# Performance work log

Measured on AMD Instinct MI355X. Metric: run time of the kernel, lower is better.

## Reference

```python
import jax, jax.numpy as jnp
import numpy as np

N_NODES = 100000
N_EDGES = 800000
VOCAB = 256      # node_dict_size
NODE_DIM = 256
HIDDEN = 256
N_MASK = 10000


def setup_inputs() -> dict:
    key = jax.random.key(0)
    ks = jax.random.split(key, 8)
    return {
        "x": jax.random.randint(ks[0], (N_NODES, 1), 0, VOCAB, dtype=jnp.int64 if jax.config.jax_enable_x64 else jnp.int32),
        "edge_index": jax.random.randint(ks[1], (2, N_EDGES), 0, N_NODES, dtype=jnp.int32),
        "mask_x_position": jax.random.randint(ks[2], (N_MASK,), 0, N_NODES, dtype=jnp.int32),
        "emb": jax.random.normal(ks[3], (VOCAB, NODE_DIM), dtype=jnp.float32) * (NODE_DIM ** -0.5),
        "W1": jax.random.normal(ks[4], (NODE_DIM, HIDDEN), dtype=jnp.float32) * (NODE_DIM ** -0.5),
        "b1": jnp.zeros((HIDDEN,), dtype=jnp.float32),
        "W2": jax.random.normal(ks[5], (HIDDEN, VOCAB), dtype=jnp.float32) * (HIDDEN ** -0.5),
        "b2": jnp.zeros((VOCAB,), dtype=jnp.float32),
    }


def _gcn_conv(h, W, b, src, dst, norm, n_nodes):
    # PyG GCNConv: out = scatter_add(norm * (h @ W)[src], dst) + b
    hw = h @ W                                      # [N, out]
    msgs = hw[src] * norm[:, None]                  # [E+N, out]
    out = jax.ops.segment_sum(msgs, dst, num_segments=n_nodes)
    return out + b


def _gcn_norm(edge_index, n_nodes):
    # add self-loops, compute sym-normalized edge weights (PyG gcn_norm)
    loops = jnp.arange(n_nodes, dtype=edge_index.dtype)
    src = jnp.concatenate([edge_index[0], loops])
    dst = jnp.concatenate([edge_index[1], loops])
    deg = jax.ops.segment_sum(jnp.ones_like(dst, dtype=jnp.float32), dst,
                              num_segments=n_nodes)  # in-degree incl. self-loop
    dinv = jnp.where(deg > 0, jax.lax.rsqrt(deg), 0.0)
    norm = dinv[src] * dinv[dst]                    # [E+N]
    return src, dst, norm


def reference(x, edge_index, mask_x_position, emb, W1, b1, W2, b2):
    n_nodes = x.shape[0]
    src, dst, norm = _gcn_norm(edge_index, n_nodes)
    h = emb[x[:, 0]]                                # Embedding + squeeze(1) -> [N, node_dim]
    # dropout p=0 / eval mode -> identity
    h = _gcn_conv(h, W1, b1, src, dst, norm, n_nodes)
    h = jax.nn.relu(h)
    h = _gcn_conv(h, W2, b2, src, dst, norm, n_nodes)  # [N, vocab]
    return jax.nn.log_softmax(h[mask_x_position], axis=1)
```

## Files before the change

### kernel.cpp

```cpp
#include <hip/hip_runtime.h>
#include <stdint.h>

#define NN 100000
#define NE 800000
#define ND 256
#define NM 10000
#define NMP 10048
#define NTOT (NN + NM)
#define NTB ((NTOT + 1023) / 1024)
#define NPB 128
#define NBK 782
#define BCAP 1280
#define TILE 1024
#define EBK ((NE + TILE - 1) / TILE)

typedef __attribute__((ext_vector_type(8))) short bf16x8;
typedef __attribute__((ext_vector_type(4))) float f32x4;

__device__ __forceinline__ float bf2f(unsigned short u) {
    return __uint_as_float(((unsigned)u) << 16);
}
__device__ __forceinline__ unsigned short f2bf(float f) {
    unsigned u = __float_as_uint(f);
    u += 0x7fffu + ((u >> 16) & 1u);
    return (unsigned short)(u >> 16);
}


__global__ void k_maskmap(const int* __restrict__ mpos, int* __restrict__ minfo,
                          int* __restrict__ flag, int* __restrict__ gcur,
                          int* __restrict__ nctr) {
    int j = blockIdx.x * 256 + threadIdx.x;
    if (j < NM) {
        int p = mpos[j];
        minfo[p] = (j + 1) << 1;
        flag[p] = 1;
    }
    if (j < NBK) gcur[j] = j * BCAP;
    if (j == 0) *nctr = 0;
}

__global__ __launch_bounds__(256) void k_bin(
    const int* __restrict__ src, const int* __restrict__ dst,
    const int* __restrict__ minfo, int* __restrict__ flag,
    int* __restrict__ gcur, int* __restrict__ ebuf,
    const float* __restrict__ emb, const float* __restrict__ W1,
    const float* __restrict__ W2,
    unsigned short* __restrict__ M1, unsigned short* __restrict__ W2t) {
    __shared__ int lcnt[NBK];
    __shared__ int sd[TILE], ss[TILE];
    __shared__ float er[ND];
    int b = blockIdx.x, t = threadIdx.x;
    if (b >= EBK) {
        int bb = b - EBK;
        if (bb < ND) {
            er[t] = emb[bb * ND + t];
            __syncthreads();
            float acc = 0.f;
            for (int k = 0; k < ND; k++) acc += er[k] * W1[k * ND + t];
            M1[bb * ND + t] = f2bf(acc);
        } else {
            int n = bb - ND;
            W2t[n * ND + t] = f2bf(W2[t * ND + n]);
        }
        return;
    }
    for (int i = t; i < NBK; i += 256) lcnt[i] = 0;
    __syncthreads();
    int e0 = b * TILE;
#pragma unroll
    for (int k = 0; k < TILE / 256; k++) {
        int idx = t + k * 256;
        int e = e0 + idx;
        if (e < NE) {
            int d = dst[e], s = src[e];
            sd[idx] = d; ss[idx] = s;
            atomicAdd(&lcnt[d >> 7], 1);
            if (minfo[d] > 0) atomicExch(&flag[s], 1);
        }
    }
    __syncthreads();
    for (int i = t; i < NBK; i += 256) {
        int c = lcnt[i];
        lcnt[i] = c ? atomicAdd(&gcur[i], c) : 0;
    }
    __syncthreads();
    int nv = min(NE - e0, TILE);
#pragma unroll
    for (int k = 0; k < TILE / 256; k++) {
        int idx = t + k * 256;
        if (idx < nv) {
            int d = sd[idx], s = ss[idx];
            int bk = d >> 7, j = d & 127;
            int pos = atomicAdd(&lcnt[bk], 1);
            if (pos < (bk + 1) * BCAP) ebuf[pos] = s | (j << 17);
        }
    }
}

__global__ void k_bhist(const int* __restrict__ gcur, const int* __restrict__ ebuf,
                        int* __restrict__ carr) {
    __shared__ int bins[NPB];
    int b = blockIdx.x, t = threadIdx.x;
    if (t < NPB) bins[t] = 0;
    __syncthreads();
    int n = min(gcur[b] - b * BCAP, BCAP);
    int base = b * BCAP;
    for (int i = t; i < n; i += 256)
        atomicAdd(&bins[ebuf[base + i] >> 17], 1);
    __syncthreads();
    int node = b * NPB + t;
    if (t < NPB && node < NN) carr[node] = bins[t];
}

__global__ void k_scanA(int* __restrict__ carr, int* __restrict__ part,
                        const int* __restrict__ x, const int* __restrict__ flag,
                        const int* __restrict__ mpos,
                        int4* __restrict__ xd4,
                        int* __restrict__ nctr, int* __restrict__ nlist) {
    int b = blockIdx.x, t = threadIdx.x;
    int base = b * 1024 + t * 4;
    int s = 0;
#pragma unroll
    for (int k = 0; k < 4; k++) {
        int i = base + k;
        if (i < NTOT) {
            int c;
            if (i < NN) {
                c = carr[i];
                float dv = rsqrtf((float)c + 1.0f);
                int cc = 0;
                if (flag[i] == 1) {
                    cc = atomicAdd(nctr, 1);
                    nlist[cc] = i;
                }
                xd4[i] = make_int4(x[i], __float_as_int(dv), cc, 0);
            } else {
                c = carr[mpos[i - NN]];
                carr[i] = c;
            }
            s += c;
        }
    }
    int lane = t & 63, wv = t >> 6;
    int xx = s;
    for (int o = 1; o < 64; o <<= 1) { int y = __shfl_up(xx, o, 64); if (lane >= o) xx += y; }
    __shared__ int ws[4];
    if (lane == 63) ws[wv] = xx;
    __syncthreads();
    if (t == 0) part[b] = ws[0] + ws[1] + ws[2] + ws[3];
}

__global__ void k_scanC(const int* __restrict__ carr, const int* __restrict__ part,
                        int* __restrict__ off) {
    int b = blockIdx.x, t = threadIdx.x;
    int lane = t & 63, wv = t >> 6;
    int pv = (t < b) ? part[t] : 0;
#pragma unroll
    for (int o = 32; o >= 1; o >>= 1) pv += __shfl_xor(pv, o, 64);
    __shared__ int bsum[4];
    if (lane == 0) bsum[wv] = pv;
    int base = b * 1024 + t * 4;
    int v[4]; int s = 0;
#pragma unroll
    for (int k = 0; k < 4; k++) {
        int i = base + k;
        v[k] = (i < NTOT) ? carr[i] : 0;
        s += v[k];
    }
    int xx = s;
    for (int o = 1; o < 64; o <<= 1) { int y = __shfl_up(xx, o, 64); if (lane >= o) xx += y; }
    __shared__ int ws[4];
    if (lane == 63) ws[wv] = xx;
    __syncthreads();
    int add = bsum[0] + bsum[1] + bsum[2] + bsum[3];
    for (int k = 0; k < wv; k++) add += ws[k];
    int run = add + xx - s;
#pragma unroll
    for (int k = 0; k < 4; k++) {
        int i = base + k;
        if (i < NTOT) off[i] = run;
        run += v[k];
    }
}

__global__ __launch_bounds__(256) void k_place(
    const int* __restrict__ gcur, const int* __restrict__ ebuf,
    const int* __restrict__ minfo, const int* __restrict__ flag,
    const int* __restrict__ off,
    const int4* __restrict__ xd4, int2* __restrict__ pairs) {
    __shared__ int sinfo[NPB], lc1[NPB], lc2[NPB];
    int b = blockIdx.x, t = threadIdx.x;
    if (t < NPB) {
        int node = b * NPB + t;
        int m = 0, f = 0;
        if (node < NN) {
            int mv = minfo[node];
            if (mv > 0) m = mv;
            f = (flag[node] == 1);
        }
        sinfo[t] = m | f;
        lc1[t] = (node < NN) ? off[node] : 0;
        lc2[t] = (m > 0) ? off[NN + (m >> 1) - 1] : 0;
    }
    __syncthreads();
    int n = min(gcur[b] - b * BCAP, BCAP);
    int base = b * BCAP;
    for (int i = t; i < n; i += 256) {
        int w = ebuf[base + i];
        int j = w >> 17, s = w & 0x1FFFF;
        int ii = sinfo[j];
        if (ii == 0) continue;
        int4 xv = xd4[s];
        if (ii & 1) {
            int p = atomicAdd(&lc1[j], 1);
            pairs[p] = make_int2(xv.x, xv.y);
        }
        if (ii > 1) {
            int p = atomicAdd(&lc2[j], 1);
            pairs[p] = make_int2(xv.z, xv.y);
        }
    }
}

__global__ void k_expand(const int* __restrict__ nctr, const int* __restrict__ nlist,
                         const int4* __restrict__ xd4,
                         const int* __restrict__ off, const int* __restrict__ carr,
                         const int2* __restrict__ pairs,
                         const unsigned short* __restrict__ M1,
                         const float* __restrict__ b1,
                         unsigned short* __restrict__ h1c) {
    int lane = threadIdx.x & 63;
    int wave = (blockIdx.x * 256 + threadIdx.x) >> 6;
    if (wave >= *nctr) return;
    int i = nlist[wave];
    float4 b1v = ((const float4*)b1)[lane];
    int4 x0 = xd4[i];
    int v0 = x0.x;
    float w0 = __int_as_float(x0.y);
    ushort4 mm = *(const ushort4*)(M1 + (size_t)v0 * ND + lane * 4);
    float a0 = w0 * bf2f(mm.x), a1 = w0 * bf2f(mm.y);
    float a2 = w0 * bf2f(mm.z), a3 = w0 * bf2f(mm.w);
    int e = off[i], end = e + carr[i];
    for (; e + 4 <= end; e += 4) {
        int2 pA = pairs[e + 0];
        int2 pB = pairs[e + 1];
        int2 pC = pairs[e + 2];
        int2 pD = pairs[e + 3];
        ushort4 mA = *(const ushort4*)(M1 + (size_t)pA.x * ND + lane * 4);
        ushort4 mB = *(const ushort4*)(M1 + (size_t)pB.x * ND + lane * 4);
        ushort4 mC = *(const ushort4*)(M1 + (size_t)pC.x * ND + lane * 4);
        ushort4 mD = *(const ushort4*)(M1 + (size_t)pD.x * ND + lane * 4);
        float wA = __int_as_float(pA.y), wB = __int_as_float(pB.y);
        float wC = __int_as_float(pC.y), wD = __int_as_float(pD.y);
        a0 += wA * bf2f(mA.x) + wB * bf2f(mB.x) + wC * bf2f(mC.x) + wD * bf2f(mD.x);
        a1 += wA * bf2f(mA.y) + wB * bf2f(mB.y) + wC * bf2f(mC.y) + wD * bf2f(mD.y);
        a2 += wA * bf2f(mA.z) + wB * bf2f(mB.z) + wC * bf2f(mC.z) + wD * bf2f(mD.z);
        a3 += wA * bf2f(mA.w) + wB * bf2f(mB.w) + wC * bf2f(mC.w) + wD * bf2f(mD.w);
    }
    for (; e < end; e++) {
        int2 p = pairs[e];
        float w = __int_as_float(p.y);
        ushort4 m2 = *(const ushort4*)(M1 + (size_t)p.x * ND + lane * 4);
        a0 += w * bf2f(m2.x);
        a1 += w * bf2f(m2.y);
        a2 += w * bf2f(m2.z);
        a3 += w * bf2f(m2.w);
    }
    ushort4 o;
    o.x = f2bf(fmaxf(fmaf(w0, a0, b1v.x), 0.f));
    o.y = f2bf(fmaxf(fmaf(w0, a1, b1v.y), 0.f));
    o.z = f2bf(fmaxf(fmaf(w0, a2, b1v.z), 0.f));
    o.w = f2bf(fmaxf(fmaf(w0, a3, b1v.w), 0.f));
    ((ushort4*)(h1c + (size_t)wave * ND))[lane] = o;
}

__global__ void k_agg2(const int* __restrict__ mpos, const int* __restrict__ minfo,
                       const int4* __restrict__ xd4,
                       const int2* __restrict__ pairs, const int* __restrict__ off,
                       const int* __restrict__ carr,
                       const unsigned short* __restrict__ h1c,
                       unsigned short* __restrict__ agg2b) {
    int lane = threadIdx.x & 63;
    int wave = (blockIdx.x * 256 + threadIdx.x) >> 6;
    if (wave >= NM) return;
    int r = wave;
    int p = mpos[r];
    if ((minfo[p] >> 1) != r + 1) return;
    int4 xp = xd4[p];
    int cp = xp.z;
    float dv = __int_as_float(xp.y);
    ushort4 h0 = *(const ushort4*)(h1c + (size_t)cp * ND + lane * 4);
    float a0 = dv * bf2f(h0.x), a1 = dv * bf2f(h0.y);
    float a2 = dv * bf2f(h0.z), a3 = dv * bf2f(h0.w);
    int e = off[NN + r], end = e + carr[NN + r];
    for (; e + 4 <= end; e += 4) {
        int2 pA = pairs[e + 0];
        int2 pB = pairs[e + 1];
        int2 pC = pairs[e + 2];
        int2 pD = pairs[e + 3];
        ushort4 hA = *(const ushort4*)(h1c + (size_t)pA.x * ND + lane * 4);
        ushort4 hB = *(const ushort4*)(h1c + (size_t)pB.x * ND + lane * 4);
        ushort4 hC = *(const ushort4*)(h1c + (size_t)pC.x * ND + lane * 4);
        ushort4 hD = *(const ushort4*)(h1c + (size_t)pD.x * ND + lane * 4);
        float wA = __int_as_float(pA.y), wB = __int_as_float(pB.y);
        float wC = __int_as_float(pC.y), wD = __int_as_float(pD.y);
        a0 += wA * bf2f(hA.x) + wB * bf2f(hB.x) + wC * bf2f(hC.x) + wD * bf2f(hD.x);
        a1 += wA * bf2f(hA.y) + wB * bf2f(hB.y) + wC * bf2f(hC.y) + wD * bf2f(hD.y);
        a2 += wA * bf2f(hA.z) + wB * bf2f(hB.z) + wC * bf2f(hC.z) + wD * bf2f(hD.z);
        a3 += wA * bf2f(hA.w) + wB * bf2f(hB.w) + wC * bf2f(hC.w) + wD * bf2f(hD.w);
    }
    for (; e < end; e++) {
        int2 pp = pairs[e];
        float w = __int_as_float(pp.y);
        ushort4 hv = *(const ushort4*)(h1c + (size_t)pp.x * ND + lane * 4);
        a0 += w * bf2f(hv.x);
        a1 += w * bf2f(hv.y);
        a2 += w * bf2f(hv.z);
        a3 += w * bf2f(hv.w);
    }
    ushort4 o;
    o.x = f2bf(dv * a0);
    o.y = f2bf(dv * a1);
    o.z = f2bf(dv * a2);
    o.w = f2bf(dv * a3);
    ((ushort4*)(agg2b + (size_t)r * ND))[lane] = o;
}

__global__ __launch_bounds__(256) void k_out2(
    const int* __restrict__ mpos, const int* __restrict__ minfo,
    const unsigned short* __restrict__ agg2b, const unsigned short* __restrict__ W2t,
    const float* __restrict__ b2, float* __restrict__ out) {
    int lane = threadIdx.x & 63;
    int wv = threadIdx.x >> 6;
    int row0 = blockIdx.x * 64 + wv * 16;
    int qm = lane & 15, qk = lane >> 4;
    int row = row0 + qm;
    bf16x8 afr[8];
    if (row < NM) {
        int p = mpos[row];
        int rr = (minfo[p] >> 1) - 1;
        const unsigned short* arow = agg2b + (size_t)rr * ND + qk * 8;
#pragma unroll
        for (int kt = 0; kt < 8; kt++) afr[kt] = *(const bf16x8*)(arow + kt * 32);
    } else {
#pragma unroll
        for (int kt = 0; kt < 8; kt++) afr[kt] = (bf16x8){0, 0, 0, 0, 0, 0, 0, 0};
    }
    f32x4 acc[16];
#pragma unroll
    for (int t = 0; t < 16; t++) acc[t] = (f32x4){0.f, 0.f, 0.f, 0.f};
#pragma unroll
    for (int t = 0; t < 16; t++) {
        const unsigned short* brow = W2t + (size_t)(t * 16 + qm) * ND + qk * 8;
#pragma unroll
        for (int kt = 0; kt < 8; kt++) {
            bf16x8 bfr = *(const bf16x8*)(brow + kt * 32);
            acc[t] = __builtin_amdgcn_mfma_f32_16x16x32_bf16(afr[kt], bfr, acc[t], 0, 0, 0);
        }
    }
    float mx[4] = {-1e30f, -1e30f, -1e30f, -1e30f};
#pragma unroll
    for (int t = 0; t < 16; t++) {
        float cb = b2[qm + 16 * t];
#pragma unroll
        for (int r = 0; r < 4; r++) {
            float v = acc[t][r] + cb;
            acc[t][r] = v;
            mx[r] = fmaxf(mx[r], v);
        }
    }
#pragma unroll
    for (int r = 0; r < 4; r++)
        for (int o = 1; o < 16; o <<= 1) mx[r] = fmaxf(mx[r], __shfl_xor(mx[r], o, 64));
    float sm[4] = {0.f, 0.f, 0.f, 0.f};
#pragma unroll
    for (int t = 0; t < 16; t++)
#pragma unroll
        for (int r = 0; r < 4; r++) sm[r] += __expf(acc[t][r] - mx[r]);
#pragma unroll
    for (int r = 0; r < 4; r++)
        for (int o = 1; o < 16; o <<= 1) sm[r] += __shfl_xor(sm[r], o, 64);
#pragma unroll
    for (int r = 0; r < 4; r++) {
        int orow_i = row0 + qk * 4 + r;
        if (orow_i >= NM) continue;
        float lse = mx[r] + __logf(sm[r]);
        float* orow = out + (size_t)orow_i * ND + qm;
#pragma unroll
        for (int t = 0; t < 16; t++) orow[16 * t] = acc[t][r] - lse;
    }
}

extern "C" void kernel_launch(void* const* d_in, const int* in_sizes, int n_in,
                              void* d_out, int out_size, void* d_ws, size_t ws_size,
                              hipStream_t stream) {
    const int* x    = (const int*)d_in[0];
    const int* ei   = (const int*)d_in[1];
    const int* src  = ei;
    const int* dst  = ei + NE;
    const int* mpos = (const int*)d_in[2];
    const float* emb = (const float*)d_in[3];
    const float* W1  = (const float*)d_in[4];
    const float* b1  = (const float*)d_in[5];
    const float* W2  = (const float*)d_in[6];
    const float* b2  = (const float*)d_in[7];
    float* out = (float*)d_out;

    char* w = (char*)d_ws;
    size_t o = 0;
    int*   carr  = (int*)(w + o);  o += (size_t)(NTOT + 64) * 4;
    int*   off   = (int*)(w + o);  o += (size_t)(NTOT + 64) * 4;
    int*   minfo = (int*)(w + o);  o += (size_t)NN * 4;
    int*   flag  = (int*)(w + o);  o += (size_t)NN * 4;
    int4*  xd4   = (int4*)(w + o); o += (size_t)NN * 16;
    int*   nlist = (int*)(w + o);  o += (size_t)NN * 4;
    int*   nctr  = (int*)(w + o);  o += 64;
    int*   part  = (int*)(w + o);  o += 128 * 4;
    int*   gcur  = (int*)(w + o);  o += (size_t)(NBK + 64) * 4;
    int*   ebuf  = (int*)(w + o);  o += (size_t)NBK * BCAP * 4;
    unsigned short* M1    = (unsigned short*)(w + o); o += (size_t)ND * ND * 2;
    unsigned short* W2t   = (unsigned short*)(w + o); o += (size_t)ND * ND * 2;
    unsigned short* agg2b = (unsigned short*)(w + o); o += (size_t)NM * ND * 2;
    int2*  pairs = (int2*)(w + o); o += (size_t)NE * 2 * 8;
    unsigned short* h1c  = (unsigned short*)(w + o); o += (size_t)NN * ND * 2;

    k_maskmap<<<(NM + 255) / 256, 256, 0, stream>>>(mpos, minfo, flag, gcur, nctr);
    k_bin<<<EBK + 2 * ND, 256, 0, stream>>>(src, dst, minfo, flag, gcur, ebuf,
                                            emb, W1, W2, M1, W2t);
    k_bhist<<<NBK, 256, 0, stream>>>(gcur, ebuf, carr);
    k_scanA<<<NTB, 256, 0, stream>>>(carr, part, x, flag, mpos, xd4, nctr, nlist);
    k_scanC<<<NTB, 256, 0, stream>>>(carr, part, off);
    k_place<<<NBK, 256, 0, stream>>>(gcur, ebuf, minfo, flag, off, xd4, pairs);
    k_expand<<<(NN + 3) / 4, 256, 0, stream>>>(nctr, nlist, xd4, off, carr, pairs, M1, b1, h1c);
    k_agg2<<<(NM + 3) / 4, 256, 0, stream>>>(mpos, minfo, xd4, pairs, off, carr, h1c, agg2b);
    k_out2<<<NMP / 64, 256, 0, stream>>>(mpos, minfo, agg2b, W2t, b2, out);
}
```

Baseline: 212.5 us.

## Fuse preprocessing kernels into one cooperative persistent kernel with grid syncs

Merges the six preprocessing launches (mask map, edge binning, bucket histogram, two scan passes, pair placement) into a single cooperative kernel of 768 persistent blocks separated by grid-wide syncs. The aim is to remove per-launch overhead and inter-kernel gaps on these short phases. In exchange, blocks loop over the work, occupancy is capped by launch_bounds(256,3) with a large shared-memory footprint, and each grid sync has its own cost. Launch fails if 768 blocks cannot be co-resident.

After: 632.6 us. 198% more time.

```diff
diff --git a/kernel.cpp b/kernel.cpp
--- a/kernel.cpp
+++ b/kernel.cpp
@@ -1,5 +1,8 @@
 #include <hip/hip_runtime.h>
+#include <hip/hip_cooperative_groups.h>
 #include <stdint.h>
+
+namespace cg = cooperative_groups;
 
 #define NN 100000
 #define NE 800000
@@ -13,6 +16,7 @@
 #define BCAP 1280
 #define TILE 1024
 #define EBK ((NE + TILE - 1) / TILE)
+#define NBLK 768
 
 typedef __attribute__((ext_vector_type(8))) short bf16x8;
 typedef __attribute__((ext_vector_type(4))) float f32x4;
@@ -27,199 +31,195 @@
 }
 
 
-__global__ void k_maskmap(const int* __restrict__ mpos, int* __restrict__ minfo,
-                          int* __restrict__ flag, int* __restrict__ gcur,
-                          int* __restrict__ nctr) {
-    int j = blockIdx.x * 256 + threadIdx.x;
-    if (j < NM) {
-        int p = mpos[j];
-        minfo[p] = (j + 1) << 1;
-        flag[p] = 1;
-    }
-    if (j < NBK) gcur[j] = j * BCAP;
-    if (j == 0) *nctr = 0;
-}
-
-__global__ __launch_bounds__(256) void k_bin(
+__global__ __launch_bounds__(256, 3) void k_prep(
     const int* __restrict__ src, const int* __restrict__ dst,
-    const int* __restrict__ minfo, int* __restrict__ flag,
-    int* __restrict__ gcur, int* __restrict__ ebuf,
+    const int* __restrict__ x, const int* __restrict__ mpos,
     const float* __restrict__ emb, const float* __restrict__ W1,
     const float* __restrict__ W2,
-    unsigned short* __restrict__ M1, unsigned short* __restrict__ W2t) {
+    int* __restrict__ carr, int* __restrict__ off,
+    int* __restrict__ minfo, int* __restrict__ flag,
+    int4* __restrict__ xd4, int* __restrict__ nlist, int* __restrict__ nctr,
+    int* __restrict__ part, int* __restrict__ gcur, int* __restrict__ ebuf,
+    unsigned short* __restrict__ M1, unsigned short* __restrict__ W2t,
+    int2* __restrict__ pairs) {
+    cg::grid_group gg = cg::this_grid();
     __shared__ int lcnt[NBK];
     __shared__ int sd[TILE], ss[TILE];
     __shared__ float er[ND];
-    int b = blockIdx.x, t = threadIdx.x;
-    if (b >= EBK) {
-        int bb = b - EBK;
+    __shared__ int bins[NPB];
+    __shared__ int sinfo[NPB], lc1[NPB], lc2[NPB];
+    __shared__ int ws[4], bsum[4];
+    const int t = threadIdx.x;
+    const int lane = t & 63, wv = t >> 6;
+    const int gidx = blockIdx.x * 256 + t;
+
+    if (gidx < NM) {
+        int p = mpos[gidx];
+        minfo[p] = (gidx + 1) << 1;
+        flag[p] = 1;
+    }
+    if (gidx < NBK) gcur[gidx] = gidx * BCAP;
+    if (gidx == 0) *nctr = 0;
+    gg.sync();
+
+    for (int tile = blockIdx.x; tile < EBK; tile += NBLK) {
+        for (int i = t; i < NBK; i += 256) lcnt[i] = 0;
+        __syncthreads();
+        int e0 = tile * TILE;
+#pragma unroll
+        for (int k = 0; k < TILE / 256; k++) {
+            int idx = t + k * 256;
+            int e = e0 + idx;
+            if (e < NE) {
+                int d = dst[e], s = src[e];
+                sd[idx] = d; ss[idx] = s;
+                atomicAdd(&lcnt[d >> 7], 1);
+                if (minfo[d] > 0) atomicExch(&flag[s], 1);
+            }
+        }
+        __syncthreads();
+        for (int i = t; i < NBK; i += 256) {
+            int c = lcnt[i];
+            lcnt[i] = c ? atomicAdd(&gcur[i], c) : 0;
+        }
+        __syncthreads();
+        int nv = min(NE - e0, TILE);
+#pragma unroll
+        for (int k = 0; k < TILE / 256; k++) {
+            int idx = t + k * 256;
+            if (idx < nv) {
+                int d = sd[idx], s = ss[idx];
+                int bk = d >> 7, j = d & 127;
+                int pos = atomicAdd(&lcnt[bk], 1);
+                if (pos < (bk + 1) * BCAP) ebuf[pos] = s | (j << 17);
+            }
+        }
+        __syncthreads();
+    }
+    for (int bb = blockIdx.x; bb < 2 * ND; bb += NBLK) {
         if (bb < ND) {
             er[t] = emb[bb * ND + t];
             __syncthreads();
             float acc = 0.f;
             for (int k = 0; k < ND; k++) acc += er[k] * W1[k * ND + t];
             M1[bb * ND + t] = f2bf(acc);
+            __syncthreads();
         } else {
             int n = bb - ND;
             W2t[n * ND + t] = f2bf(W2[t * ND + n]);
         }
-        return;
-    }
-    for (int i = t; i < NBK; i += 256) lcnt[i] = 0;
-    __syncthreads();
-    int e0 = b * TILE;
-#pragma unroll
-    for (int k = 0; k < TILE / 256; k++) {
-        int idx = t + k * 256;
-        int e = e0 + idx;
-        if (e < NE) {
-            int d = dst[e], s = src[e];
-            sd[idx] = d; ss[idx] = s;
-            atomicAdd(&lcnt[d >> 7], 1);
-            if (minfo[d] > 0) atomicExch(&flag[s], 1);
-        }
-    }
-    __syncthreads();
-    for (int i = t; i < NBK; i += 256) {
-        int c = lcnt[i];
-        lcnt[i] = c ? atomicAdd(&gcur[i], c) : 0;
-    }
-    __syncthreads();
-    int nv = min(NE - e0, TILE);
-#pragma unroll
-    for (int k = 0; k < TILE / 256; k++) {
-        int idx = t + k * 256;
-        if (idx < nv) {
-            int d = sd[idx], s = ss[idx];
-            int bk = d >> 7, j = d & 127;
-            int pos = atomicAdd(&lcnt[bk], 1);
-            if (pos < (bk + 1) * BCAP) ebuf[pos] = s | (j << 17);
-        }
-    }
-}
-
-__global__ void k_bhist(const int* __restrict__ gcur, const int* __restrict__ ebuf,
-                        int* __restrict__ carr) {
-    __shared__ int bins[NPB];
-    int b = blockIdx.x, t = threadIdx.x;
-    if (t < NPB) bins[t] = 0;
-    __syncthreads();
-    int n = min(gcur[b] - b * BCAP, BCAP);
-    int base = b * BCAP;
-    for (int i = t; i < n; i += 256)
-        atomicAdd(&bins[ebuf[base + i] >> 17], 1);
-    __syncthreads();
-    int node = b * NPB + t;
-    if (t < NPB && node < NN) carr[node] = bins[t];
-}
-
-__global__ void k_scanA(int* __restrict__ carr, int* __restrict__ part,
-                        const int* __restrict__ x, const int* __restrict__ flag,
-                        const int* __restrict__ mpos,
-                        int4* __restrict__ xd4,
-                        int* __restrict__ nctr, int* __restrict__ nlist) {
-    int b = blockIdx.x, t = threadIdx.x;
-    int base = b * 1024 + t * 4;
-    int s = 0;
-#pragma unroll
-    for (int k = 0; k < 4; k++) {
-        int i = base + k;
-        if (i < NTOT) {
-            int c;
-            if (i < NN) {
-                c = carr[i];
-                float dv = rsqrtf((float)c + 1.0f);
-                int cc = 0;
-                if (flag[i] == 1) {
-                    cc = atomicAdd(nctr, 1);
-                    nlist[cc] = i;
+    }
+    gg.sync();
+
+    for (int b = blockIdx.x; b < NBK; b += NBLK) {
+        if (t < NPB) bins[t] = 0;
+        __syncthreads();
+        int n = min(gcur[b] - b * BCAP, BCAP);
+        int base = b * BCAP;
+        for (int i = t; i < n; i += 256)
+            atomicAdd(&bins[ebuf[base + i] >> 17], 1);
+        __syncthreads();
+        int node = b * NPB + t;
+        if (t < NPB && node < NN) carr[node] = bins[t];
+        __syncthreads();
+    }
+    gg.sync();
+
+    for (int b = blockIdx.x; b < NTB; b += NBLK) {
+        int base = b * 1024 + t * 4;
+        int s = 0;
+#pragma unroll
+        for (int k = 0; k < 4; k++) {
+            int i = base + k;
+            if (i < NTOT) {
+                int c;
+                if (i < NN) {
+                    c = carr[i];
+                    float dv = rsqrtf((float)c + 1.0f);
+                    int cc = 0;
+                    if (flag[i] == 1) {
+                        cc = atomicAdd(nctr, 1);
+                        nlist[cc] = i;
+                    }
+                    xd4[i] = make_int4(x[i], __float_as_int(dv), cc, 0);
+                } else {
+                    c = carr[mpos[i - NN]];
+                    carr[i] = c;
                 }
-                xd4[i] = make_int4(x[i], __float_as_int(dv), cc, 0);
-            } else {
-                c = carr[mpos[i - NN]];
-                carr[i] = c;
-            }
-            s += c;
-        }
-    }
-    int lane = t & 63, wv = t >> 6;
-    int xx = s;
-    for (int o = 1; o < 64; o <<= 1) { int y = __shfl_up(xx, o, 64); if (lane >= o) xx += y; }
-    __shared__ int ws[4];
-    if (lane == 63) ws[wv] = xx;
-    __syncthreads();
-    if (t == 0) part[b] = ws[0] + ws[1] + ws[2] + ws[3];
-}
-
-__global__ void k_scanC(const int* __restrict__ carr, const int* __restrict__ part,
-                        int* __restrict__ off) {
-    int b = blockIdx.x, t = threadIdx.x;
-    int lane = t & 63, wv = t >> 6;
-    int pv = (t < b) ? part[t] : 0;
-#pragma unroll
-    for (int o = 32; o >= 1; o >>= 1) pv += __shfl_xor(pv, o, 64);
-    __shared__ int bsum[4];
-    if (lane == 0) bsum[wv] = pv;
-    int base = b * 1024 + t * 4;
-    int v[4]; int s = 0;
-#pragma unroll
-    for (int k = 0; k < 4; k++) {
-        int i = base + k;
-        v[k] = (i < NTOT) ? carr[i] : 0;
-        s += v[k];
-    }
-    int xx = s;
-    for (int o = 1; o < 64; o <<= 1) { int y = __shfl_up(xx, o, 64); if (lane >= o) xx += y; }
-    __shared__ int ws[4];
-    if (lane == 63) ws[wv] = xx;
-    __syncthreads();
-    int add = bsum[0] + bsum[1] + bsum[2] + bsum[3];
-    for (int k = 0; k < wv; k++) add += ws[k];
-    int run = add + xx - s;
-#pragma unroll
-    for (int k = 0; k < 4; k++) {
-        int i = base + k;
-        if (i < NTOT) off[i] = run;
-        run += v[k];
-    }
-}
-
-__global__ __launch_bounds__(256) void k_place(
-    const int* __restrict__ gcur, const int* __restrict__ ebuf,
-    const int* __restrict__ minfo, const int* __restrict__ flag,
-    const int* __restrict__ off,
-    const int4* __restrict__ xd4, int2* __restrict__ pairs) {
-    __shared__ int sinfo[NPB], lc1[NPB], lc2[NPB];
-    int b = blockIdx.x, t = threadIdx.x;
-    if (t < NPB) {
-        int node = b * NPB + t;
-        int m = 0, f = 0;
-        if (node < NN) {
-            int mv = minfo[node];
-            if (mv > 0) m = mv;
-            f = (flag[node] == 1);
-        }
-        sinfo[t] = m | f;
-        lc1[t] = (node < NN) ? off[node] : 0;
-        lc2[t] = (m > 0) ? off[NN + (m >> 1) - 1] : 0;
-    }
-    __syncthreads();
-    int n = min(gcur[b] - b * BCAP, BCAP);
-    int base = b * BCAP;
-    for (int i = t; i < n; i += 256) {
-        int w = ebuf[base + i];
-        int j = w >> 17, s = w & 0x1FFFF;
-        int ii = sinfo[j];
-        if (ii == 0) continue;
-        int4 xv = xd4[s];
-        if (ii & 1) {
-            int p = atomicAdd(&lc1[j], 1);
-            pairs[p] = make_int2(xv.x, xv.y);
-        }
-        if (ii > 1) {
-            int p = atomicAdd(&lc2[j], 1);
-            pairs[p] = make_int2(xv.z, xv.y);
-        }
+                s += c;
+            }
+        }
+        int xx = s;
+        for (int o = 1; o < 64; o <<= 1) { int y = __shfl_up(xx, o, 64); if (lane >= o) xx += y; }
+        if (lane == 63) ws[wv] = xx;
+        __syncthreads();
+        if (t == 0) part[b] = ws[0] + ws[1] + ws[2] + ws[3];
+        __syncthreads();
+    }
+    gg.sync();
+
+    for (int b = blockIdx.x; b < NTB; b += NBLK) {
+        int pv = (t < b) ? part[t] : 0;
+#pragma unroll
+        for (int o = 32; o >= 1; o >>= 1) pv += __shfl_xor(pv, o, 64);
+        if (lane == 0) bsum[wv] = pv;
+        int base = b * 1024 + t * 4;
+        int v[4]; int s = 0;
+#pragma unroll
+        for (int k = 0; k < 4; k++) {
+            int i = base + k;
+            v[k] = (i < NTOT) ? carr[i] : 0;
+            s += v[k];
+        }
+        int xx = s;
+        for (int o = 1; o < 64; o <<= 1) { int y = __shfl_up(xx, o, 64); if (lane >= o) xx += y; }
+        if (lane == 63) ws[wv] = xx;
+        __syncthreads();
+        int add = bsum[0] + bsum[1] + bsum[2] + bsum[3];
+        for (int k = 0; k < wv; k++) add += ws[k];
+        int run = add + xx - s;
+#pragma unroll
+        for (int k = 0; k < 4; k++) {
+            int i = base + k;
+            if (i < NTOT) off[i] = run;
+            run += v[k];
+        }
+        __syncthreads();
+    }
+    gg.sync();
+
+    for (int b = blockIdx.x; b < NBK; b += NBLK) {
+        if (t < NPB) {
+            int node = b * NPB + t;
+            int m = 0, f = 0;
+            if (node < NN) {
+                int mv = minfo[node];
+                if (mv > 0) m = mv;
+                f = (flag[node] == 1);
+            }
+            sinfo[t] = m | f;
+            lc1[t] = (node < NN) ? off[node] : 0;
+            lc2[t] = (m > 0) ? off[NN + (m >> 1) - 1] : 0;
+        }
+        __syncthreads();
+        int n = min(gcur[b] - b * BCAP, BCAP);
+        int base = b * BCAP;
+        for (int i = t; i < n; i += 256) {
+            int w = ebuf[base + i];
+            int j = w >> 17, s = w & 0x1FFFF;
+            int ii = sinfo[j];
+            if (ii == 0) continue;
+            int4 xv = xd4[s];
+            if (ii & 1) {
+                int p = atomicAdd(&lc1[j], 1);
+                pairs[p] = make_int2(xv.x, xv.y);
+            }
+            if (ii > 1) {
+                int p = atomicAdd(&lc2[j], 1);
+                pairs[p] = make_int2(xv.z, xv.y);
+            }
+        }
+        __syncthreads();
     }
 }
 
@@ -425,13 +425,12 @@
     int2*  pairs = (int2*)(w + o); o += (size_t)NE * 2 * 8;
     unsigned short* h1c  = (unsigned short*)(w + o); o += (size_t)NN * ND * 2;
 
-    k_maskmap<<<(NM + 255) / 256, 256, 0, stream>>>(mpos, minfo, flag, gcur, nctr);
-    k_bin<<<EBK + 2 * ND, 256, 0, stream>>>(src, dst, minfo, flag, gcur, ebuf,
-                                            emb, W1, W2, M1, W2t);
-    k_bhist<<<NBK, 256, 0, stream>>>(gcur, ebuf, carr);
-    k_scanA<<<NTB, 256, 0, stream>>>(carr, part, x, flag, mpos, xd4, nctr, nlist);
-    k_scanC<<<NTB, 256, 0, stream>>>(carr, part, off);
-    k_place<<<NBK, 256, 0, stream>>>(gcur, ebuf, minfo, flag, off, xd4, pairs);
+    void* args[] = {(void*)&src, (void*)&dst, (void*)&x, (void*)&mpos, (void*)&emb,
+                    (void*)&W1, (void*)&W2,
+                    (void*)&carr, (void*)&off, (void*)&minfo, (void*)&flag, (void*)&xd4,
+                    (void*)&nlist, (void*)&nctr, (void*)&part, (void*)&gcur, (void*)&ebuf,
+                    (void*)&M1, (void*)&W2t, (void*)&pairs};
+    hipLaunchCooperativeKernel((const void*)k_prep, dim3(NBLK), dim3(256), args, 0, stream);
     k_expand<<<(NN + 3) / 4, 256, 0, stream>>>(nctr, nlist, xd4, off, carr, pairs, M1, b1, h1c);
     k_agg2<<<(NM + 3) / 4, 256, 0, stream>>>(mpos, minfo, xd4, pairs, off, carr, h1c, agg2b);
     k_out2<<<NMP / 64, 256, 0, stream>>>(mpos, minfo, agg2b, W2t, b2, out);
```

## Fuse degree scan into bhist/place and use byte flags for mask membership

Applied to the files above, without the earlier changes.

Folds the per-node work from the old scanA into k_bhist and adds a per-bucket partial sum there. A tiny single-block k_scanB then scans the 782 bucket partials, and k_place derives per-node offsets itself. This replaces two grid-wide scan kernels over NN+NM entries with one small scan, and duplicate mask positions now share each node's second pair segment instead of getting separate ones. The int flag arrays become byte arrays, and the atomicExch is replaced by a plain byte store, which cuts traffic and atomics in the edge-binning pass. The cost is a barrier inside divergent branches in k_place and a few more serial dependencies between launches.

After: 209.4 us. Within noise of the previous version (-1.4%).

```diff
diff --git a/kernel.cpp b/kernel.cpp
--- a/kernel.cpp
+++ b/kernel.cpp
@@ -6,8 +6,6 @@
 #define ND 256
 #define NM 10000
 #define NMP 10048
-#define NTOT (NN + NM)
-#define NTB ((NTOT + 1023) / 1024)
 #define NPB 128
 #define NBK 782
 #define BCAP 1280
@@ -28,13 +26,14 @@
 
 
 __global__ void k_maskmap(const int* __restrict__ mpos, int* __restrict__ minfo,
-                          int* __restrict__ flag, int* __restrict__ gcur,
-                          int* __restrict__ nctr) {
+                          unsigned char* __restrict__ mb, unsigned char* __restrict__ fb,
+                          int* __restrict__ gcur, int* __restrict__ nctr) {
     int j = blockIdx.x * 256 + threadIdx.x;
     if (j < NM) {
         int p = mpos[j];
         minfo[p] = (j + 1) << 1;
-        flag[p] = 1;
+        mb[p] = 1;
+        fb[p] = 1;
     }
     if (j < NBK) gcur[j] = j * BCAP;
     if (j == 0) *nctr = 0;
@@ -42,7 +41,7 @@
 
 __global__ __launch_bounds__(256) void k_bin(
     const int* __restrict__ src, const int* __restrict__ dst,
-    const int* __restrict__ minfo, int* __restrict__ flag,
+    const unsigned char* __restrict__ mb, unsigned char* __restrict__ fb,
     int* __restrict__ gcur, int* __restrict__ ebuf,
     const float* __restrict__ emb, const float* __restrict__ W1,
     const float* __restrict__ W2,
@@ -76,7 +75,7 @@
             int d = dst[e], s = src[e];
             sd[idx] = d; ss[idx] = s;
             atomicAdd(&lcnt[d >> 7], 1);
-            if (minfo[d] > 0) atomicExch(&flag[s], 1);
+            if (mb[d] == 1) fb[s] = 1;
         }
     }
     __syncthreads();
@@ -99,9 +98,15 @@
 }
 
 __global__ void k_bhist(const int* __restrict__ gcur, const int* __restrict__ ebuf,
-                        int* __restrict__ carr) {
+                        const int* __restrict__ x, const unsigned char* __restrict__ mb,
+                        const unsigned char* __restrict__ fb,
+                        int* __restrict__ carr, int4* __restrict__ xd4,
+                        int* __restrict__ nlist, int* __restrict__ nctr,
+                        int* __restrict__ part) {
     __shared__ int bins[NPB];
+    __shared__ int rs[4];
     int b = blockIdx.x, t = threadIdx.x;
+    int lane = t & 63, wv = t >> 6;
     if (t < NPB) bins[t] = 0;
     __syncthreads();
     int n = min(gcur[b] - b * BCAP, BCAP);
@@ -110,98 +115,82 @@
         atomicAdd(&bins[ebuf[base + i] >> 17], 1);
     __syncthreads();
     int node = b * NPB + t;
-    if (t < NPB && node < NN) carr[node] = bins[t];
-}
-
-__global__ void k_scanA(int* __restrict__ carr, int* __restrict__ part,
-                        const int* __restrict__ x, const int* __restrict__ flag,
-                        const int* __restrict__ mpos,
-                        int4* __restrict__ xd4,
-                        int* __restrict__ nctr, int* __restrict__ nlist) {
-    int b = blockIdx.x, t = threadIdx.x;
-    int base = b * 1024 + t * 4;
-    int s = 0;
+    int w = 0;
+    if (t < NPB && node < NN) {
+        int c = bins[t];
+        carr[node] = c;
+        float dv = rsqrtf((float)c + 1.0f);
+        int cc = 0;
+        if (fb[node] == 1) {
+            cc = atomicAdd(nctr, 1);
+            nlist[cc] = node;
+        }
+        xd4[node] = make_int4(x[node], __float_as_int(dv), cc, 0);
+        w = c + ((mb[node] == 1) ? c : 0);
+    }
+#pragma unroll
+    for (int o = 32; o >= 1; o >>= 1) w += __shfl_xor(w, o, 64);
+    if (lane == 0) rs[wv] = w;
+    __syncthreads();
+    if (t == 0) part[b] = rs[0] + rs[1] + rs[2] + rs[3];
+}
+
+__global__ void k_scanB(int* __restrict__ part) {
+    int t = threadIdx.x;
+    int lane = t & 63, wv = t >> 6;
+    int base = t * 4;
+    int v[4]; int s = 0;
 #pragma unroll
     for (int k = 0; k < 4; k++) {
-        int i = base + k;
-        if (i < NTOT) {
-            int c;
-            if (i < NN) {
-                c = carr[i];
-                float dv = rsqrtf((float)c + 1.0f);
-                int cc = 0;
-                if (flag[i] == 1) {
-                    cc = atomicAdd(nctr, 1);
-                    nlist[cc] = i;
-                }
-                xd4[i] = make_int4(x[i], __float_as_int(dv), cc, 0);
-            } else {
-                c = carr[mpos[i - NN]];
-                carr[i] = c;
-            }
-            s += c;
-        }
-    }
-    int lane = t & 63, wv = t >> 6;
+        v[k] = (base + k < NBK) ? part[base + k] : 0;
+        s += v[k];
+    }
     int xx = s;
     for (int o = 1; o < 64; o <<= 1) { int y = __shfl_up(xx, o, 64); if (lane >= o) xx += y; }
     __shared__ int ws[4];
     if (lane == 63) ws[wv] = xx;
     __syncthreads();
-    if (t == 0) part[b] = ws[0] + ws[1] + ws[2] + ws[3];
-}
-
-__global__ void k_scanC(const int* __restrict__ carr, const int* __restrict__ part,
-                        int* __restrict__ off) {
+    int add = 0;
+    for (int k = 0; k < wv; k++) add += ws[k];
+    int run = add + xx - s;
+#pragma unroll
+    for (int k = 0; k < 4; k++) {
+        if (base + k < NBK) part[base + k] = run;
+        run += v[k];
+    }
+}
+
+__global__ __launch_bounds__(256) void k_place(
+    const int* __restrict__ gcur, const int* __restrict__ ebuf,
+    const int* __restrict__ minfo, const unsigned char* __restrict__ fb,
+    const int* __restrict__ carr, const int* __restrict__ part,
+    const int4* __restrict__ xd4, int* __restrict__ off, int2* __restrict__ pairs) {
+    __shared__ int sinfo[NPB], lc1[NPB], lc2[NPB];
+    __shared__ int wtot[2];
     int b = blockIdx.x, t = threadIdx.x;
     int lane = t & 63, wv = t >> 6;
-    int pv = (t < b) ? part[t] : 0;
-#pragma unroll
-    for (int o = 32; o >= 1; o >>= 1) pv += __shfl_xor(pv, o, 64);
-    __shared__ int bsum[4];
-    if (lane == 0) bsum[wv] = pv;
-    int base = b * 1024 + t * 4;
-    int v[4]; int s = 0;
-#pragma unroll
-    for (int k = 0; k < 4; k++) {
-        int i = base + k;
-        v[k] = (i < NTOT) ? carr[i] : 0;
-        s += v[k];
-    }
-    int xx = s;
-    for (int o = 1; o < 64; o <<= 1) { int y = __shfl_up(xx, o, 64); if (lane >= o) xx += y; }
-    __shared__ int ws[4];
-    if (lane == 63) ws[wv] = xx;
-    __syncthreads();
-    int add = bsum[0] + bsum[1] + bsum[2] + bsum[3];
-    for (int k = 0; k < wv; k++) add += ws[k];
-    int run = add + xx - s;
-#pragma unroll
-    for (int k = 0; k < 4; k++) {
-        int i = base + k;
-        if (i < NTOT) off[i] = run;
-        run += v[k];
-    }
-}
-
-__global__ __launch_bounds__(256) void k_place(
-    const int* __restrict__ gcur, const int* __restrict__ ebuf,
-    const int* __restrict__ minfo, const int* __restrict__ flag,
-    const int* __restrict__ off,
-    const int4* __restrict__ xd4, int2* __restrict__ pairs) {
-    __shared__ int sinfo[NPB], lc1[NPB], lc2[NPB];
-    int b = blockIdx.x, t = threadIdx.x;
     if (t < NPB) {
         int node = b * NPB + t;
-        int m = 0, f = 0;
+        int c = 0, m = 0, f = 0;
         if (node < NN) {
+            c = carr[node];
             int mv = minfo[node];
             if (mv > 0) m = mv;
-            f = (flag[node] == 1);
-        }
+            f = (fb[node] == 1) ? 1 : 0;
+        }
+        int w = c + (m ? c : 0);
+        int xx = w;
+        for (int o = 1; o < 64; o <<= 1) { int y = __shfl_up(xx, o, 64); if (lane >= o) xx += y; }
+        if (lane == 63) wtot[wv] = xx;
+        __syncthreads();
+        int excl = xx - w + ((wv == 1) ? wtot[0] : 0);
+        int myoff = part[b] + excl;
+        if (node < NN) off[node] = myoff;
         sinfo[t] = m | f;
-        lc1[t] = (node < NN) ? off[node] : 0;
-        lc2[t] = (m > 0) ? off[NN + (m >> 1) - 1] : 0;
+        lc1[t] = myoff;
+        lc2[t] = myoff + c;
+    } else {
+        __syncthreads();
     }
     __syncthreads();
     int n = min(gcur[b] - b * BCAP, BCAP);
@@ -293,7 +282,8 @@
     ushort4 h0 = *(const ushort4*)(h1c + (size_t)cp * ND + lane * 4);
     float a0 = dv * bf2f(h0.x), a1 = dv * bf2f(h0.y);
     float a2 = dv * bf2f(h0.z), a3 = dv * bf2f(h0.w);
-    int e = off[NN + r], end = e + carr[NN + r];
+    int c2 = carr[p];
+    int e = off[p] + c2, end = e + c2;
     for (; e + 4 <= end; e += 4) {
         int2 pA = pairs[e + 0];
         int2 pB = pairs[e + 1];
@@ -409,14 +399,15 @@
 
     char* w = (char*)d_ws;
     size_t o = 0;
-    int*   carr  = (int*)(w + o);  o += (size_t)(NTOT + 64) * 4;
-    int*   off   = (int*)(w + o);  o += (size_t)(NTOT + 64) * 4;
+    int*   carr  = (int*)(w + o);  o += (size_t)(NN + 64) * 4;
+    int*   off   = (int*)(w + o);  o += (size_t)(NN + 64) * 4;
     int*   minfo = (int*)(w + o);  o += (size_t)NN * 4;
-    int*   flag  = (int*)(w + o);  o += (size_t)NN * 4;
+    unsigned char* mb = (unsigned char*)(w + o); o += (size_t)(NN + 64);
+    unsigned char* fb = (unsigned char*)(w + o); o += (size_t)(NN + 64);
     int4*  xd4   = (int4*)(w + o); o += (size_t)NN * 16;
     int*   nlist = (int*)(w + o);  o += (size_t)NN * 4;
     int*   nctr  = (int*)(w + o);  o += 64;
-    int*   part  = (int*)(w + o);  o += 128 * 4;
+    int*   part  = (int*)(w + o);  o += 1024 * 4;
     int*   gcur  = (int*)(w + o);  o += (size_t)(NBK + 64) * 4;
     int*   ebuf  = (int*)(w + o);  o += (size_t)NBK * BCAP * 4;
     unsigned short* M1    = (unsigned short*)(w + o); o += (size_t)ND * ND * 2;
@@ -425,13 +416,12 @@
     int2*  pairs = (int2*)(w + o); o += (size_t)NE * 2 * 8;
     unsigned short* h1c  = (unsigned short*)(w + o); o += (size_t)NN * ND * 2;
 
-    k_maskmap<<<(NM + 255) / 256, 256, 0, stream>>>(mpos, minfo, flag, gcur, nctr);
-    k_bin<<<EBK + 2 * ND, 256, 0, stream>>>(src, dst, minfo, flag, gcur, ebuf,
+    k_maskmap<<<(NM + 255) / 256, 256, 0, stream>>>(mpos, minfo, mb, fb, gcur, nctr);
+    k_bin<<<EBK + 2 * ND, 256, 0, stream>>>(src, dst, mb, fb, gcur, ebuf,
                                             emb, W1, W2, M1, W2t);
-    k_bhist<<<NBK, 256, 0, stream>>>(gcur, ebuf, carr);
-    k_scanA<<<NTB, 256, 0, stream>>>(carr, part, x, flag, mpos, xd4, nctr, nlist);
-    k_scanC<<<NTB, 256, 0, stream>>>(carr, part, off);
-    k_place<<<NBK, 256, 0, stream>>>(gcur, ebuf, minfo, flag, off, xd4, pairs);
+    k_bhist<<<NBK, 256, 0, stream>>>(gcur, ebuf, x, mb, fb, carr, xd4, nlist, nctr, part);
+    k_scanB<<<1, 256, 0, stream>>>(part);
+    k_place<<<NBK, 256, 0, stream>>>(gcur, ebuf, minfo, fb, carr, part, xd4, off, pairs);
     k_expand<<<(NN + 3) / 4, 256, 0, stream>>>(nctr, nlist, xd4, off, carr, pairs, M1, b1, h1c);
     k_agg2<<<(NM + 3) / 4, 256, 0, stream>>>(mpos, minfo, xd4, pairs, off, carr, h1c, agg2b);
     k_out2<<<NMP / 64, 256, 0, stream>>>(mpos, minfo, agg2b, W2t, b2, out);
```
